# Optimization experiments

Measured on AMD Instinct MI355X. Metric: run time of the kernel, lower is better.

The kernel has to match this reference:

```python
import jax, jax.numpy as jnp
import numpy as np

N = 8192       # nodes
IN_F = 512     # in_features
OUT_F = 256    # out_features


def setup_inputs() -> dict:
    key = jax.random.key(0)
    k1, k2, k3, k4 = jax.random.split(key, 4)
    # xavier_uniform-like scales for params
    w_scale = 1.414 * (6.0 / (IN_F + OUT_F)) ** 0.5
    a_scale = 1.414 * (6.0 / (2 * OUT_F + 1)) ** 0.5
    x = jax.random.normal(k1, (N, IN_F), jnp.float32)
    W = jax.random.uniform(k2, (IN_F, OUT_F), jnp.float32, -w_scale, w_scale)
    a = jax.random.uniform(k3, (2 * OUT_F, 1), jnp.float32, -a_scale, a_scale)
    adj = jax.random.randint(k4, (N, N), 0, 2, jnp.int32)
    return {"x": x, "W": W, "a": a, "adj": adj}


def reference(x, W, a, adj):
    # h = x @ W : [N, OUT_F]
    h = x @ W
    f = W.shape[1]
    a1, a2 = a[:f], a[f:]          # each [OUT_F, 1]
    # Original builds a_input[i,j] = concat(h_i, h_j) then matmuls with a.
    # Equivalent decomposition: e[i,j] = h_i . a1 + h_j . a2
    e = (h @ a1) + (h @ a2).T      # [N, N]
    neg = jnp.float32(-9e15)
    attention = jnp.where(adj > 0, e, neg)   # no softmax in the original
    h_prime = attention @ h        # [N, OUT_F]
    return h_prime
```

## Files before the change

### kernel.cpp

```cpp
#include <hip/hip_runtime.h>


#define NEG_BIG (-9000000000000000.0f)

typedef __bf16 bf16x8 __attribute__((ext_vector_type(8)));
typedef float f32x16 __attribute__((ext_vector_type(16)));

static __device__ __forceinline__ unsigned short f2bf(float f) {
  unsigned u = __builtin_bit_cast(unsigned, f);
  u = u + 0x7FFFu + ((u >> 16) & 1u);
  return (unsigned short)(u >> 16);
}
static __device__ __forceinline__ float bfbits2f(unsigned hi16) {
  return __builtin_bit_cast(float, hi16 << 16);
}
static __device__ __forceinline__ unsigned pk2(float a, float b) {
  return (unsigned)f2bf(a) | ((unsigned)f2bf(b) << 16);
}
static __device__ __forceinline__ bf16x8 asbf(int4 q) {
  return __builtin_bit_cast(bf16x8, q);
}
static __device__ __forceinline__ f32x16 mfma(bf16x8 a, int4 b, f32x16 c) {
  return __builtin_amdgcn_mfma_f32_32x32x16_bf16(a, asbf(b), c, 0, 0, 0);
}

__global__ __launch_bounds__(256) void k0_bits(const int* __restrict__ adj,
    unsigned long long* __restrict__ bm) {
  const int w = threadIdx.x >> 6, l = threadIdx.x & 63;
  const int row = blockIdx.x * 4 + w;
  const int4* ar = (const int4*)(adj + (size_t)row * 8192) + l;
  unsigned long long* br = bm + (size_t)row * 128;
#pragma unroll 2
  for (int b = 0; b < 32; ++b) {
    int4 v = ar[b * 64];
    unsigned long long b0 = __ballot(v.x > 0);
    unsigned long long b1 = __ballot(v.y > 0);
    unsigned long long b2 = __ballot(v.z > 0);
    unsigned long long b3 = __ballot(v.w > 0);
    if (l == 0) {
      ulonglong2* p = (ulonglong2*)(br + (size_t)b * 4);
      p[0] = make_ulonglong2(b0, b1);
      p[1] = make_ulonglong2(b2, b3);
    }
  }
}

__global__ void k1a_wt(const float* __restrict__ W, unsigned short* __restrict__ WT,
                       float* __restrict__ T) {
  const int i = blockIdx.x * 256 + threadIdx.x;
  const int k = i >> 8, n = i & 255;
  WT[n * 512 + k] = f2bf(W[i]);
  if (blockIdx.x == 0) T[threadIdx.x] = 0.f;
}

__global__ __launch_bounds__(256) void k1b_h(const float* __restrict__ x,
    const unsigned short* __restrict__ WT, unsigned short* __restrict__ hP) {
  __shared__ unsigned short XS[64 * 264];
  const int t = threadIdx.x;
  const int mt = blockIdx.x;
  const int m0 = mt << 5;
  const int row = t >> 3, c7 = t & 7;
  const float* xr = x + (size_t)(m0 + row) * 512 + c7 * 4;
  const int gb = c7 >> 1, off = (t & 1) * 4;
#pragma unroll
  for (int j = 0; j < 16; ++j) {
    float4 v = *(const float4*)(xr + 32 * j);
    *(uint2*)&XS[(gb + 4 * j) * 264 + row * 8 + off] =
        make_uint2(pk2(v.x, v.y), pk2(v.z, v.w));
  }
  __syncthreads();
  const int w = t >> 6, l = t & 63, l31 = l & 31, lh = l >> 5;
  f32x16 acc0, acc1;
  for (int i = 0; i < 16; ++i) { acc0[i] = 0.f; acc1[i] = 0.f; }
  const int nt0 = w * 2;
  const unsigned short* w0 = WT + (size_t)(nt0 * 32 + l31) * 512 + lh * 8;
  const unsigned short* w1 = w0 + 32 * 512;
  const char* XB = (const char*)XS + lh * 528 + l31 * 16;
#pragma unroll 4
  for (int ks = 0; ks < 32; ++ks) {
    bf16x8 Af = *(const bf16x8*)(XB + ks * 1056);
    int4 b0 = *(const int4*)(w0 + ks * 16);
    int4 b1 = *(const int4*)(w1 + ks * 16);
    acc0 = mfma(Af, b0, acc0);
    acc1 = mfma(Af, b1, acc1);
  }
#pragma unroll
  for (int reg = 0; reg < 16; ++reg) {
    const int mm = (reg & 3) + 8 * (reg >> 2) + 4 * lh;
    const int sl = ((mm >> 1) & 1) * 16 + (mm & 1) * 8 + (mm >> 2);
    hP[(size_t)mt * 8192 + (nt0 * 32 + l31) * 32 + sl] = f2bf(acc0[reg]);
    hP[(size_t)mt * 8192 + ((nt0 + 1) * 32 + l31) * 32 + sl] = f2bf(acc1[reg]);
  }
}

__global__ __launch_bounds__(256) void k2_colsum(const unsigned short* __restrict__ hP,
                                                 float* __restrict__ T) {
  const int t = threadIdx.x;
  const int b = blockIdx.x;
  const int4* p = (const int4*)(hP + (size_t)b * 8192 + t * 32);
  int4 q0 = p[0], q1 = p[1], q2 = p[2], q3 = p[3];
  float s = 0.f;
  const unsigned* u0 = (const unsigned*)&q0;
  const unsigned* u1 = (const unsigned*)&q1;
  const unsigned* u2 = (const unsigned*)&q2;
  const unsigned* u3 = (const unsigned*)&q3;
#pragma unroll
  for (int i = 0; i < 4; ++i) {
    s += bfbits2f(u0[i] & 0xFFFFu) + bfbits2f(u0[i] >> 16);
    s += bfbits2f(u1[i] & 0xFFFFu) + bfbits2f(u1[i] >> 16);
    s += bfbits2f(u2[i] & 0xFFFFu) + bfbits2f(u2[i] >> 16);
    s += bfbits2f(u3[i] & 0xFFFFu) + bfbits2f(u3[i] >> 16);
  }
  atomicAdd(&T[t], s);
}

__global__ __launch_bounds__(256, 2) void k3_att(
    const unsigned long long* __restrict__ bm,
    const unsigned short* __restrict__ hP, const float* __restrict__ T,
    float* __restrict__ out) {
  __shared__ float red[3][64][64];
  const int t = threadIdx.x, blk = blockIdx.x;
  const int w = t >> 6, l = t & 63, l31 = l & 31, lh = l >> 5;
  const int s = w;
  const int rb = blk >> 2, cb = blk & 3;
  const int r0 = rb * 64;
  const int cw0 = cb * 64;

  const char* bmr0 = (const char*)bm + (size_t)(r0 + l31) * 1024 + s * 256 + lh * 8;
  const char* bmr1 = bmr0 + 32 * 1024;
  const unsigned short* hB = hP + (size_t)(cw0 + l31) * 32 + lh * 8;

  f32x16 acc[2][2];
#pragma unroll
  for (int mt = 0; mt < 2; ++mt)
#pragma unroll
    for (int nt = 0; nt < 2; ++nt)
#pragma unroll
      for (int i = 0; i < 16; ++i) acc[mt][nt][i] = 0.f;

  uint2 pA0a, pA0b, pA1a, pA1b, pB0a, pB0b, pB1a, pB1b;
  int4 BvA[4], BvB[4];
  int jt = s * 64;

#define LOADBM(k, A0a, A0b, A1a, A1b)                                       \
  A0a = *(const uint2*)(bmr0 + (k) * 32);                                   \
  A0b = *(const uint2*)(bmr0 + (k) * 32 + 16);                              \
  A1a = *(const uint2*)(bmr1 + (k) * 32);                                   \
  A1b = *(const uint2*)(bmr1 + (k) * 32 + 16);

#define XP(dw, m3, u4)                                                      \
  {                                                                         \
    const unsigned bb_ = ((dw) >> (8 * (m3))) & 0xFFu;                      \
    const unsigned tt_ = bb_ | (bb_ << 15);                                 \
    u4.x = ((tt_)&0x00010001u) * 0x3F80u;                                   \
    u4.y = ((tt_ >> 2) & 0x00010001u) * 0x3F80u;                            \
    u4.z = ((tt_ >> 4) & 0x00010001u) * 0x3F80u;                            \
    u4.w = ((tt_ >> 6) & 0x00010001u) * 0x3F80u;                            \
  }

#define ITER(mm, A0a, A0b, A1a, A1b, BVC, BVN)                              \
  {                                                                         \
    {                                                                       \
      const unsigned short* hb_ = hB + (size_t)(jt + 1) * 8192;             \
      BVN[0] = *(const int4*)(hb_);                                         \
      BVN[1] = *(const int4*)(hb_ + 16);                                    \
      BVN[2] = *(const int4*)(hb_ + 1024);                                  \
      BVN[3] = *(const int4*)(hb_ + 1040);                                  \
    }                                                                       \
    const unsigned d00_ = ((mm) >> 2) ? A0a.y : A0a.x;         \
    const unsigned d01_ = ((mm) >> 2) ? A0b.y : A0b.x;         \
    const unsigned d10_ = ((mm) >> 2) ? A1a.y : A1a.x;         \
    const unsigned d11_ = ((mm) >> 2) ? A1b.y : A1b.x;         \
    uint4 u00_, u01_, u10_, u11_;                                           \
    XP(d00_, (mm)&3, u00_)                                                  \
    XP(d01_, (mm)&3, u01_)                                                  \
    XP(d10_, (mm)&3, u10_)                                                  \
    XP(d11_, (mm)&3, u11_)                                                  \
    const bf16x8 A00_ = __builtin_bit_cast(bf16x8, u00_);                   \
    const bf16x8 A01_ = __builtin_bit_cast(bf16x8, u01_);                   \
    const bf16x8 A10_ = __builtin_bit_cast(bf16x8, u10_);                   \
    const bf16x8 A11_ = __builtin_bit_cast(bf16x8, u11_);                   \
    acc[0][0] = mfma(A00_, BVC[0], acc[0][0]);                              \
    acc[1][0] = mfma(A10_, BVC[0], acc[1][0]);                              \
    acc[0][1] = mfma(A00_, BVC[2], acc[0][1]);                              \
    acc[1][1] = mfma(A10_, BVC[2], acc[1][1]);                              \
    acc[0][0] = mfma(A01_, BVC[1], acc[0][0]);                              \
    acc[1][0] = mfma(A11_, BVC[1], acc[1][0]);                              \
    acc[0][1] = mfma(A01_, BVC[3], acc[0][1]);                              \
    acc[1][1] = mfma(A11_, BVC[3], acc[1][1]);                              \
    ++jt;                                                                   \
  }

  LOADBM(0, pA0a, pA0b, pA1a, pA1b)
  {
    const unsigned short* hb_ = hB + (size_t)jt * 8192;
    BvA[0] = *(const int4*)(hb_);
    BvA[1] = *(const int4*)(hb_ + 16);
    BvA[2] = *(const int4*)(hb_ + 1024);
    BvA[3] = *(const int4*)(hb_ + 1040);
  }

#pragma unroll 1
  for (int b2 = 0; b2 < 8; b2 += 2) {
    LOADBM(b2 + 1, pB0a, pB0b, pB1a, pB1b)
    ITER(0, pA0a, pA0b, pA1a, pA1b, BvA, BvB)
    ITER(1, pA0a, pA0b, pA1a, pA1b, BvB, BvA)
    ITER(2, pA0a, pA0b, pA1a, pA1b, BvA, BvB)
    ITER(3, pA0a, pA0b, pA1a, pA1b, BvB, BvA)
    ITER(4, pA0a, pA0b, pA1a, pA1b, BvA, BvB)
    ITER(5, pA0a, pA0b, pA1a, pA1b, BvB, BvA)
    ITER(6, pA0a, pA0b, pA1a, pA1b, BvA, BvB)
    ITER(7, pA0a, pA0b, pA1a, pA1b, BvB, BvA)
    if (b2 + 2 < 8) { LOADBM(b2 + 2, pA0a, pA0b, pA1a, pA1b) }
    ITER(0, pB0a, pB0b, pB1a, pB1b, BvA, BvB)
    ITER(1, pB0a, pB0b, pB1a, pB1b, BvB, BvA)
    ITER(2, pB0a, pB0b, pB1a, pB1b, BvA, BvB)
    ITER(3, pB0a, pB0b, pB1a, pB1b, BvB, BvA)
    ITER(4, pB0a, pB0b, pB1a, pB1b, BvA, BvB)
    ITER(5, pB0a, pB0b, pB1a, pB1b, BvB, BvA)
    ITER(6, pB0a, pB0b, pB1a, pB1b, BvA, BvB)
    ITER(7, pB0a, pB0b, pB1a, pB1b, BvB, BvA)
  }
#undef ITER
#undef XP
#undef LOADBM

  if (s > 0) {
#pragma unroll
    for (int mt = 0; mt < 2; ++mt)
#pragma unroll
      for (int nt = 0; nt < 2; ++nt)
#pragma unroll
        for (int reg = 0; reg < 16; ++reg)
          red[s - 1][(mt * 2 + nt) * 16 + reg][l] = acc[mt][nt][reg];
  }
  __syncthreads();
  if (s == 0) {
#pragma unroll
    for (int mt = 0; mt < 2; ++mt)
#pragma unroll
      for (int nt = 0; nt < 2; ++nt) {
        const int cc = cw0 + nt * 32 + l31;
        const float tv = T[cc];
#pragma unroll
        for (int reg = 0; reg < 16; ++reg) {
          const int idx = (mt * 2 + nt) * 16 + reg;
          const float am = acc[mt][nt][reg] + red[0][idx][l] +
                           red[1][idx][l] + red[2][idx][l];
          const int rr = r0 + mt * 32 + (reg & 3) + 8 * (reg >> 2) + 4 * lh;
          out[(size_t)rr * 256 + cc] = NEG_BIG * (tv - am);
        }
      }
  }
}

extern "C" void kernel_launch(void* const* d_in, const int* in_sizes, int n_in,
                              void* d_out, int out_size, void* d_ws, size_t ws_size,
                              hipStream_t stream) {
  const float* x = (const float*)d_in[0];
  const float* W = (const float*)d_in[1];
  const int* adj = (const int*)d_in[3];
  float* out = (float*)d_out;
  char* ws = (char*)d_ws;
  unsigned short* WT = (unsigned short*)(ws);
  unsigned short* hP = (unsigned short*)(ws + (1 << 20));
  float* T = (float*)(ws + (6 << 20));
  unsigned long long* bm = (unsigned long long*)(ws + (8 << 20));

  k0_bits<<<2048, 256, 0, stream>>>(adj, bm);
  k1a_wt<<<512, 256, 0, stream>>>(W, WT, T);
  k1b_h<<<256, 256, 0, stream>>>(x, WT, hP);
  k2_colsum<<<256, 256, 0, stream>>>(hP, T);
  k3_att<<<512, 256, 0, stream>>>(bm, hP, T, out);
}
```

Measured before the change: 441.3 us.

## Deepen global-load prefetch pipeline in attention kernel with explicit vmcnt waits

Replaces the compiler-scheduled double-buffered loads of the h panel and adjacency bitmask with inline-asm global loads into four rotating register stages, gated by explicit s_waitcnt vmcnt counters and sched barriers. The aim is to keep more memory requests in flight per wave and hide global-load latency behind the MFMA work. In exchange it uses more VGPRs for the extra stages, which may affect occupancy at the 2-blocks-per-CU launch bound. Hand-counted vmcnt values are fragile if the load order changes. The loads past the last tile may read beyond the used range.

```diff
diff --git a/kernel.cpp b/kernel.cpp
--- a/kernel.cpp
+++ b/kernel.cpp
@@ -126,9 +126,13 @@
   const int r0 = rb * 64;
   const int cw0 = cb * 64;
 
-  const char* bmr0 = (const char*)bm + (size_t)(r0 + l31) * 1024 + s * 256 + lh * 8;
-  const char* bmr1 = bmr0 + 32 * 1024;
-  const unsigned short* hB = hP + (size_t)(cw0 + l31) * 32 + lh * 8;
+  const char* pM0 = (const char*)bm + (size_t)(r0 + l31) * 1024 + s * 256 + lh * 8;
+  const char* pM1 = pM0 + 32 * 1024;
+  const char* pB0 = (const char*)hP + (size_t)(cw0 + l31) * 64 + lh * 16 +
+                    (size_t)(s * 64) * 16384;
+  const char* pB1 = pB0 + 16384;
+  const char* pB2 = pB0 + 32768;
+  const char* pB3 = pB0 + 49152;
 
   f32x16 acc[2][2];
 #pragma unroll
@@ -138,16 +142,33 @@
 #pragma unroll
       for (int i = 0; i < 16; ++i) acc[mt][nt][i] = 0.f;
 
-  uint2 pA0a, pA0b, pA1a, pA1b, pB0a, pB0b, pB1a, pB1b;
-  int4 BvA[4], BvB[4];
-  int jt = s * 64;
-
-#define LOADBM(k, A0a, A0b, A1a, A1b)                                       \
-  A0a = *(const uint2*)(bmr0 + (k) * 32);                                   \
-  A0b = *(const uint2*)(bmr0 + (k) * 32 + 16);                              \
-  A1a = *(const uint2*)(bmr1 + (k) * 32);                                   \
-  A1b = *(const uint2*)(bmr1 + (k) * 32 + 16);
-
+  int4 Bv0_0, Bv0_1, Bv0_2, Bv0_3;
+  int4 Bv1_0, Bv1_1, Bv1_2, Bv1_3;
+  int4 Bv2_0, Bv2_1, Bv2_2, Bv2_3;
+  int4 Bv3_0, Bv3_1, Bv3_2, Bv3_3;
+  uint2 mA0, mA1, mA2, mA3, mB0, mB1, mB2, mB3;
+
+#define GLD16(dst, ptr, OFF)                                                \
+  asm volatile("global_load_dwordx4 %0, %1, off offset:" #OFF               \
+               : "=v"(dst) : "v"(ptr));
+#define GLD8(dst, ptr, OFF)                                                 \
+  asm volatile("global_load_dwordx2 %0, %1, off offset:" #OFF               \
+               : "=v"(dst) : "v"(ptr));
+#define STAGE_B(S)                                                          \
+  GLD16(Bv##S##_0, pB##S, 0)                                                \
+  GLD16(Bv##S##_1, pB##S, 32)                                               \
+  GLD16(Bv##S##_2, pB##S, 2048)                                             \
+  GLD16(Bv##S##_3, pB##S, 2080)                                             \
+  pB##S += 65536;
+#define STAGE_M(SET)                                                        \
+  GLD8(m##SET##0, pM0, 0)                                                   \
+  GLD8(m##SET##1, pM0, 16)                                                  \
+  GLD8(m##SET##2, pM1, 0)                                                   \
+  GLD8(m##SET##3, pM1, 16)                                                  \
+  pM0 += 32; pM1 += 32;
+#define VWAIT(K)                                                            \
+  asm volatile("s_waitcnt vmcnt(" #K ")" ::: "memory");                     \
+  __builtin_amdgcn_sched_barrier(0);
 #define XP(dw, m3, u4)                                                      \
   {                                                                         \
     const unsigned bb_ = ((dw) >> (8 * (m3))) & 0xFFu;                      \
@@ -157,73 +178,60 @@
     u4.z = ((tt_ >> 4) & 0x00010001u) * 0x3F80u;                            \
     u4.w = ((tt_ >> 6) & 0x00010001u) * 0x3F80u;                            \
   }
-
-#define ITER(mm, A0a, A0b, A1a, A1b, BVC, BVN)                              \
+#define ITER(i, S, K, C)                                                    \
+  VWAIT(K)                                                                  \
   {                                                                         \
-    {                                                                       \
-      const unsigned short* hb_ = hB + (size_t)(jt + 1) * 8192;             \
-      BVN[0] = *(const int4*)(hb_);                                         \
-      BVN[1] = *(const int4*)(hb_ + 16);                                    \
-      BVN[2] = *(const int4*)(hb_ + 1024);                                  \
-      BVN[3] = *(const int4*)(hb_ + 1040);                                  \
-    }                                                                       \
-    const unsigned d00_ = ((mm) >> 2) ? A0a.y : A0a.x;         \
-    const unsigned d01_ = ((mm) >> 2) ? A0b.y : A0b.x;         \
-    const unsigned d10_ = ((mm) >> 2) ? A1a.y : A1a.x;         \
-    const unsigned d11_ = ((mm) >> 2) ? A1b.y : A1b.x;         \
+    const uint2 c0_ = m##C##0;                                 \
+    const uint2 c1_ = m##C##1;                                 \
+    const uint2 c2_ = m##C##2;                                 \
+    const uint2 c3_ = m##C##3;                                 \
+    const unsigned d00_ = ((i) >> 2) ? c0_.y : c0_.x;                       \
+    const unsigned d01_ = ((i) >> 2) ? c1_.y : c1_.x;                       \
+    const unsigned d10_ = ((i) >> 2) ? c2_.y : c2_.x;                       \
+    const unsigned d11_ = ((i) >> 2) ? c3_.y : c3_.x;                       \
     uint4 u00_, u01_, u10_, u11_;                                           \
-    XP(d00_, (mm)&3, u00_)                                                  \
-    XP(d01_, (mm)&3, u01_)                                                  \
-    XP(d10_, (mm)&3, u10_)                                                  \
-    XP(d11_, (mm)&3, u11_)                                                  \
+    XP(d00_, (i)&3, u00_)                                                   \
+    XP(d01_, (i)&3, u01_)                                                   \
+    XP(d10_, (i)&3, u10_)                                                   \
+    XP(d11_, (i)&3, u11_)                                                   \
     const bf16x8 A00_ = __builtin_bit_cast(bf16x8, u00_);                   \
     const bf16x8 A01_ = __builtin_bit_cast(bf16x8, u01_);                   \
     const bf16x8 A10_ = __builtin_bit_cast(bf16x8, u10_);                   \
     const bf16x8 A11_ = __builtin_bit_cast(bf16x8, u11_);                   \
-    acc[0][0] = mfma(A00_, BVC[0], acc[0][0]);                              \
-    acc[1][0] = mfma(A10_, BVC[0], acc[1][0]);                              \
-    acc[0][1] = mfma(A00_, BVC[2], acc[0][1]);                              \
-    acc[1][1] = mfma(A10_, BVC[2], acc[1][1]);                              \
-    acc[0][0] = mfma(A01_, BVC[1], acc[0][0]);                              \
-    acc[1][0] = mfma(A11_, BVC[1], acc[1][0]);                              \
-    acc[0][1] = mfma(A01_, BVC[3], acc[0][1]);                              \
-    acc[1][1] = mfma(A11_, BVC[3], acc[1][1]);                              \
-    ++jt;                                                                   \
-  }
-
-  LOADBM(0, pA0a, pA0b, pA1a, pA1b)
-  {
-    const unsigned short* hb_ = hB + (size_t)jt * 8192;
-    BvA[0] = *(const int4*)(hb_);
-    BvA[1] = *(const int4*)(hb_ + 16);
-    BvA[2] = *(const int4*)(hb_ + 1024);
-    BvA[3] = *(const int4*)(hb_ + 1040);
-  }
+    acc[0][0] = mfma(A00_, Bv##S##_0, acc[0][0]);                           \
+    acc[1][0] = mfma(A10_, Bv##S##_0, acc[1][0]);                           \
+    acc[0][1] = mfma(A00_, Bv##S##_2, acc[0][1]);                           \
+    acc[1][1] = mfma(A10_, Bv##S##_2, acc[1][1]);                           \
+    acc[0][0] = mfma(A01_, Bv##S##_1, acc[0][0]);                           \
+    acc[1][0] = mfma(A11_, Bv##S##_1, acc[1][0]);                           \
+    acc[0][1] = mfma(A01_, Bv##S##_3, acc[0][1]);                           \
+    acc[1][1] = mfma(A11_, Bv##S##_3, acc[1][1]);                           \
+  }                                                                         \
+  STAGE_B(S)
+#define BLOCK(C, N)                                                         \
+  STAGE_M(N)                                                                \
+  ITER(0, 0, 16, C) ITER(1, 1, 16, C) ITER(2, 2, 16, C) ITER(3, 3, 16, C)   \
+  ITER(4, 0, 12, C) ITER(5, 1, 12, C) ITER(6, 2, 12, C) ITER(7, 3, 12, C)
+
+  STAGE_M(A)
+  STAGE_B(0) STAGE_B(1) STAGE_B(2) STAGE_B(3)
 
 #pragma unroll 1
-  for (int b2 = 0; b2 < 8; b2 += 2) {
-    LOADBM(b2 + 1, pB0a, pB0b, pB1a, pB1b)
-    ITER(0, pA0a, pA0b, pA1a, pA1b, BvA, BvB)
-    ITER(1, pA0a, pA0b, pA1a, pA1b, BvB, BvA)
-    ITER(2, pA0a, pA0b, pA1a, pA1b, BvA, BvB)
-    ITER(3, pA0a, pA0b, pA1a, pA1b, BvB, BvA)
-    ITER(4, pA0a, pA0b, pA1a, pA1b, BvA, BvB)
-    ITER(5, pA0a, pA0b, pA1a, pA1b, BvB, BvA)
-    ITER(6, pA0a, pA0b, pA1a, pA1b, BvA, BvB)
-    ITER(7, pA0a, pA0b, pA1a, pA1b, BvB, BvA)
-    if (b2 + 2 < 8) { LOADBM(b2 + 2, pA0a, pA0b, pA1a, pA1b) }
-    ITER(0, pB0a, pB0b, pB1a, pB1b, BvA, BvB)
-    ITER(1, pB0a, pB0b, pB1a, pB1b, BvB, BvA)
-    ITER(2, pB0a, pB0b, pB1a, pB1b, BvA, BvB)
-    ITER(3, pB0a, pB0b, pB1a, pB1b, BvB, BvA)
-    ITER(4, pB0a, pB0b, pB1a, pB1b, BvA, BvB)
-    ITER(5, pB0a, pB0b, pB1a, pB1b, BvB, BvA)
-    ITER(6, pB0a, pB0b, pB1a, pB1b, BvA, BvB)
-    ITER(7, pB0a, pB0b, pB1a, pB1b, BvB, BvA)
-  }
+  for (int b2 = 0; b2 < 4; ++b2) {
+    BLOCK(A, B)
+    BLOCK(B, A)
+  }
+#undef BLOCK
 #undef ITER
 #undef XP
-#undef LOADBM
+#undef VWAIT
+#undef STAGE_M
+#undef STAGE_B
+#undef GLD8
+#undef GLD16
+
+  asm volatile("s_waitcnt vmcnt(0)" ::: "memory");
+  __builtin_amdgcn_sched_barrier(0);
 
   if (s > 0) {
 #pragma unroll
```

After: 444.1 us. Within noise of the previous version (+0.6%).
